# Performance work log

Hardware: AMD Instinct MI355X
Metric: run time of the kernel (lower is better)

## Reference

```python
import jax, jax.numpy as jnp
import numpy as np
import math

B, S, DIM = 2, 2048, 2048
H, KV, HD = 16, 1, 128  # query heads, kv heads, head dim


def setup_inputs() -> dict:
    key = jax.random.key(0)
    ks = jax.random.split(key, 6)
    std = 0.02
    return {
        "hidden_states": jax.random.normal(ks[0], (B, S, DIM), jnp.float32),
        "attention_mask": jnp.zeros((B, 1, S, S), jnp.float32),
        "wq": jax.random.normal(ks[1], (DIM, H * HD), jnp.float32) * std,
        "bq": jnp.zeros((H * HD,), jnp.float32),
        "wk": jax.random.normal(ks[2], (DIM, KV * HD), jnp.float32) * std,
        "bk": jnp.zeros((KV * HD,), jnp.float32),
        "wv": jax.random.normal(ks[3], (DIM, KV * HD), jnp.float32) * std,
        "bv": jnp.zeros((KV * HD,), jnp.float32),
        "wo": jax.random.normal(ks[4], (H * HD, DIM), jnp.float32) * std,
        "bo": jnp.zeros((DIM,), jnp.float32),
    }


def reference(hidden_states, attention_mask, wq, bq, wk, bk, wv, bv, wo, bo):
    b, s, _ = hidden_states.shape
    q = (hidden_states @ wq + bq).reshape(b, s, H, HD)
    k = (hidden_states @ wk + bk).reshape(b, s, KV, HD)
    v = (hidden_states @ wv + bv).reshape(b, s, KV, HD)
    # [b, h, s, d]
    q = jnp.transpose(q, (0, 2, 1, 3))
    k = jnp.transpose(k, (0, 2, 1, 3))
    v = jnp.transpose(v, (0, 2, 1, 3))
    # broadcast shared KV heads to all query heads (num_kv_heads < num_query_heads)
    repeats = H // KV
    k = jnp.repeat(k, repeats, axis=1)
    v = jnp.repeat(v, repeats, axis=1)
    scores = jnp.einsum('bhqd,bhkd->bhqk', q, k) / math.sqrt(HD)
    scores = scores + attention_mask
    weights = jax.nn.softmax(scores, axis=-1)
    attn = jnp.einsum('bhqk,bhkd->bhqd', weights, v)
    attn = jnp.transpose(attn, (0, 2, 1, 3)).reshape(b, s, H * HD)
    return attn @ wo + bo
```

## Files before the change

kernel.cpp:

```cpp
#include <hip/hip_runtime.h>
#include <hip/hip_bf16.h>
#include <stdint.h>

#define S_LEN 2048
#define DIMSZ 2048
#define NH    16
#define HD    128
#define NQK   2176
#define NQKV  2304
#define NT2   (S_LEN / 128)

typedef short  bf16x8  __attribute__((ext_vector_type(8)));
typedef float  floatx4 __attribute__((ext_vector_type(4)));
typedef float  floatx16 __attribute__((ext_vector_type(16)));
typedef int    intx4   __attribute__((ext_vector_type(4)));
typedef unsigned short u16;

#define mfma32 __builtin_amdgcn_mfma_f32_32x32x16_bf16
#define LOG2E 1.4426950408889634f

__device__ __forceinline__ u16 f2bf(float x) {
  unsigned int u = __builtin_bit_cast(unsigned int, x);
  u = (u + 0x7FFFu + ((u >> 16) & 1u)) >> 16;
  return (u16)u;
}

__device__ __forceinline__ int cvtpk(float lo, float hi) {
  int r;
  asm("v_cvt_pk_bf16_f32 %0, %1, %2" : "=v"(r) : "v"(lo), "v"(hi));
  return r;
}

#if __has_builtin(__builtin_amdgcn_exp2f)
__device__ __forceinline__ float fexp2(float x) { return __builtin_amdgcn_exp2f(x); }
#else
__device__ __forceinline__ float fexp2(float x) { return exp2f(x); }
#endif

#if __has_builtin(__builtin_amdgcn_permlane32_swap)
__device__ __forceinline__ void half_swap(int& a, int& b) {
  auto r = __builtin_amdgcn_permlane32_swap(a, b, false, false);
  a = (int)r[0]; b = (int)r[1];
}
__device__ __forceinline__ float red_max32(float x) {
  int xi = __builtin_bit_cast(int, x);
  auto r = __builtin_amdgcn_permlane32_swap(xi, xi, false, false);
  return fmaxf(__builtin_bit_cast(float, (int)r[0]), __builtin_bit_cast(float, (int)r[1]));
}
__device__ __forceinline__ float red_add32(float x) {
  int xi = __builtin_bit_cast(int, x);
  auto r = __builtin_amdgcn_permlane32_swap(xi, xi, false, false);
  return __builtin_bit_cast(float, (int)r[0]) + __builtin_bit_cast(float, (int)r[1]);
}
#else
__device__ __forceinline__ void half_swap(int& a, int& b) {
  int as = __shfl_xor(a, 32);
  int bs = __shfl_xor(b, 32);
  int lane = threadIdx.x & 63;
  int na = (lane < 32) ? a : bs;
  int nb = (lane < 32) ? as : b;
  a = na; b = nb;
}
__device__ __forceinline__ float red_max32(float x) { return fmaxf(x, __shfl_xor(x, 32)); }
__device__ __forceinline__ float red_add32(float x) { return x + __shfl_xor(x, 32); }
#endif

__device__ __forceinline__ void gload16(const void* g, void* l) {
  __builtin_amdgcn_global_load_lds(
      reinterpret_cast<const __attribute__((address_space(1))) void*>(reinterpret_cast<uintptr_t>(g)),
      reinterpret_cast<__attribute__((address_space(3))) void*>(reinterpret_cast<uintptr_t>(l)),
      16, 0, 0);
}

__global__ void k_cvt_bf16(const float* __restrict__ in, u16* __restrict__ out, int n4) {
  int i = blockIdx.x * blockDim.x + threadIdx.x;
  if (i < n4) {
    float4 v = ((const float4*)in)[i];
    ushort4 o;
    o.x = f2bf(v.x); o.y = f2bf(v.y); o.z = f2bf(v.z); o.w = f2bf(v.w);
    ((ushort4*)out)[i] = o;
  }
}

__global__ void k_transpose_bf16(const float* __restrict__ in, u16* __restrict__ out,
                                 int K, int N, int rowOff) {
  __shared__ float t[64][65];
  int c0 = blockIdx.x * 64;
  int r0 = blockIdx.y * 64;
  int tid = threadIdx.x;
  int lr = tid >> 6;
  int lc = tid & 63;
#pragma unroll
  for (int i = 0; i < 16; ++i) {
    int r = lr + i * 4;
    t[r][lc] = in[(size_t)(r0 + r) * N + c0 + lc];
  }
  __syncthreads();
#pragma unroll
  for (int i = 0; i < 16; ++i) {
    int r = lr + i * 4;
    out[(size_t)(rowOff + c0 + r) * K + r0 + lc] = f2bf(t[lc][r]);
  }
}

__global__ void k_bias_concat(const float* __restrict__ bq, const float* __restrict__ bk,
                              const float* __restrict__ bv, float* __restrict__ out) {
  int i = blockIdx.x * 256 + threadIdx.x;
  if (i < NQKV) out[i] = (i < 2048) ? bq[i] : (i < NQK ? bk[i - 2048] : bv[i - NQK]);
}

__device__ __forceinline__ void stage_tile(const u16* __restrict__ G, int ldg, int row0, int kt,
                                           u16* lbase, int wid, int lane) {
#pragma unroll
  for (int i = 0; i < 4; ++i) {
    int c   = (wid * 4 + i) * 64 + lane;
    int row = c >> 3, cin = c & 7;
    int cs  = cin ^ (row & 7);
    const u16* g = G + (size_t)(row0 + row) * ldg + kt * 64 + cs * 8;
    gload16(g, (char*)lbase + (wid * 4 + i) * 1024);
  }
}

template <int OMODE>
__global__ __launch_bounds__(256)
void k_gemm(const u16* __restrict__ A, const u16* __restrict__ Bt,
            const float* __restrict__ bias, void* __restrict__ Cout,
            u16* __restrict__ vt, int M, int N, int K) {
  __shared__ u16 lA[2][128 * 64];
  __shared__ u16 lB[2][128 * 64];
  const int tid = threadIdx.x, lane = tid & 63, wid = tid >> 6;
  const int wm = wid >> 1, wn = wid & 1;
  const int tm = blockIdx.x, tn = blockIdx.y;
  const int nk = K >> 6;

  stage_tile(A, K, tm * 128, 0, lA[0], wid, lane);
  stage_tile(Bt, K, tn * 128, 0, lB[0], wid, lane);
  __syncthreads();

  floatx4 acc[4][4] = {};
  int buf = 0;
  for (int kt = 0; kt < nk; ++kt) {
    if (kt + 1 < nk) {
      stage_tile(A, K, tm * 128, kt + 1, lA[buf ^ 1], wid, lane);
      stage_tile(Bt, K, tn * 128, kt + 1, lB[buf ^ 1], wid, lane);
    }
    const char* pa = (const char*)&lA[buf][0];
    const char* pb = (const char*)&lB[buf][0];
#pragma unroll
    for (int kk = 0; kk < 2; ++kk) {
      bf16x8 af[4], bfr[4];
      int gch = kk * 4 + (lane >> 4);
#pragma unroll
      for (int f = 0; f < 4; ++f) {
        int ra = wm * 64 + f * 16 + (lane & 15);
        af[f]  = *(const bf16x8*)(pa + ra * 128 + ((gch ^ (ra & 7)) << 4));
        int rb = wn * 64 + f * 16 + (lane & 15);
        bfr[f] = *(const bf16x8*)(pb + rb * 128 + ((gch ^ (rb & 7)) << 4));
      }
      __builtin_amdgcn_s_setprio(1);
#pragma unroll
      for (int fm = 0; fm < 4; ++fm)
#pragma unroll
        for (int fn = 0; fn < 4; ++fn)
          acc[fm][fn] = __builtin_amdgcn_mfma_f32_16x16x32_bf16(af[fm], bfr[fn], acc[fm][fn], 0, 0, 0);
      __builtin_amdgcn_s_setprio(0);
    }
    __syncthreads();
    buf ^= 1;
  }

#pragma unroll
  for (int fm = 0; fm < 4; ++fm)
#pragma unroll
    for (int fn = 0; fn < 4; ++fn)
#pragma unroll
      for (int r = 0; r < 4; ++r) {
        int rowg = tm * 128 + wm * 64 + fm * 16 + (lane >> 4) * 4 + r;
        int colg = tn * 128 + wn * 64 + fn * 16 + (lane & 15);
        float v = acc[fm][fn][r] + bias[colg];
        if constexpr (OMODE == 1) {
          ((float*)Cout)[(size_t)rowg * N + colg] = v;
        } else {
          if (colg < NQK) {
            ((u16*)Cout)[(size_t)rowg * N + colg] = f2bf(v);
          } else {
            int d = colg - NQK;
            int bg = rowg >> 11, s = rowg & 2047;
            vt[((size_t)bg * HD + d) * S_LEN + s] = f2bf(v);
          }
        }
      }
}

__device__ __forceinline__ void stage_k128(const u16* __restrict__ qkv, int b, int kt,
                                           u16* lK, int wid, int lane) {
#pragma unroll
  for (int i = 0; i < 4; ++i) {
    int seg = wid * 4 + i;
    int r = seg * 4 + (lane >> 4);
    int cin = lane & 15;
    int cs = cin ^ (r & 15);
    const u16* g = qkv + (size_t)(b * S_LEN + kt * 128 + r) * NQKV + 2048 + cs * 8;
    gload16(g, (char*)lK + seg * 1024);
  }
}
__device__ __forceinline__ void stage_v128(const u16* __restrict__ vt, int b, int kt,
                                           u16* lV, int wid, int lane) {
#pragma unroll
  for (int i = 0; i < 4; ++i) {
    int seg = wid * 4 + i;
    int r = seg * 4 + (lane >> 4);
    int cin = lane & 15;
    int cs = cin ^ (r & 15);
    const u16* g = vt + ((size_t)b * HD + r) * S_LEN + kt * 128 + cs * 8;
    gload16(g, (char*)lV + seg * 1024);
  }
}

__global__ __launch_bounds__(512, 2)
void k_attn(const u16* __restrict__ qkv, const u16* __restrict__ vt,
            const float* __restrict__ mask, u16* __restrict__ attn) {
  __shared__ __align__(16) u16 lK[2][128 * 128];
  __shared__ __align__(16) u16 lV[2][128 * 128];
  const int tid = threadIdx.x, lane = tid & 63, wid = tid >> 6;
  const int qt = blockIdx.x, hg = blockIdx.y, b = blockIdx.z;
  const int h = hg * 8 + wid;
  const int q = lane & 31, h5 = lane >> 5;
  const float scale = 0.08838834764831845f;

  bf16x8 qf[8];
  const size_t qrow = (size_t)(b * S_LEN + qt * 32 + q);
#pragma unroll
  for (int cs = 0; cs < 8; ++cs)
    qf[cs] = *(const bf16x8*)(qkv + qrow * NQKV + h * HD + cs * 16 + h5 * 8);

  int offK[8], offV[8];
#pragma unroll
  for (int cs = 0; cs < 8; ++cs)
    offK[cs] = q * 256 + (((cs * 2 + h5) ^ (q & 15)) << 4);
#pragma unroll
  for (int hf = 0; hf < 2; ++hf)
#pragma unroll
    for (int ks = 0; ks < 4; ++ks)
      offV[hf * 4 + ks] = q * 256 + (((hf * 8 + ks * 2 + h5) ^ (q & 15)) << 4);

  const float* mptr = mask + ((size_t)b * S_LEN + qt * 32 + q) * S_LEN + h5 * 4;

  float m_ = -1e30f, l_ = 0.f;
  floatx16 acco[4] = {};

  stage_k128(qkv, b, 0, lK[0], wid, lane);
  stage_v128(vt, b, 0, lV[0], wid, lane);
  __syncthreads();

  int buf = 0;
  for (int kt = 0; kt < NT2; ++kt) {
    if (kt + 1 < NT2) {
      stage_k128(qkv, b, kt + 1, lK[buf ^ 1], wid, lane);
      stage_v128(vt, b, kt + 1, lV[buf ^ 1], wid, lane);
    }
    const char* pKb = (const char*)&lK[buf][0];
    const char* pVb = (const char*)&lV[buf][0];

#pragma unroll
    for (int half = 0; half < 2; ++half) {
      const float* mh = mptr + kt * 128 + half * 64;
      floatx4 mk[8];
#pragma unroll
      for (int kb = 0; kb < 2; ++kb)
#pragma unroll
        for (int rg = 0; rg < 4; ++rg)
          mk[kb * 4 + rg] = *(const floatx4*)(mh + kb * 32 + rg * 8);

      floatx16 accs0 = {}, accs1 = {};
      const char* pK = pKb + half * 16384;
      __builtin_amdgcn_s_setprio(1);
#pragma unroll
      for (int cs = 0; cs < 8; ++cs) {
        bf16x8 kf0 = *(const bf16x8*)(pK + offK[cs]);
        bf16x8 kf1 = *(const bf16x8*)(pK + 8192 + offK[cs]);
        accs0 = mfma32(kf0, qf[cs], accs0, 0, 0, 0);
        accs1 = mfma32(kf1, qf[cs], accs1, 0, 0, 0);
      }
      __builtin_amdgcn_s_setprio(0);

      float pr[32];
      float pm0 = -1e30f, pm1 = -1e30f, pm2 = -1e30f, pm3 = -1e30f;
#pragma unroll
      for (int kb = 0; kb < 2; ++kb)
#pragma unroll
        for (int rg = 0; rg < 4; ++rg) {
          floatx4 m4 = mk[kb * 4 + rg];
          float s0 = (kb ? accs1[rg * 4 + 0] : accs0[rg * 4 + 0]) * scale + m4[0];
          float s1 = (kb ? accs1[rg * 4 + 1] : accs0[rg * 4 + 1]) * scale + m4[1];
          float s2 = (kb ? accs1[rg * 4 + 2] : accs0[rg * 4 + 2]) * scale + m4[2];
          float s3 = (kb ? accs1[rg * 4 + 3] : accs0[rg * 4 + 3]) * scale + m4[3];
          pr[kb * 16 + rg * 4 + 0] = s0; pm0 = fmaxf(pm0, s0);
          pr[kb * 16 + rg * 4 + 1] = s1; pm1 = fmaxf(pm1, s1);
          pr[kb * 16 + rg * 4 + 2] = s2; pm2 = fmaxf(pm2, s2);
          pr[kb * 16 + rg * 4 + 3] = s3; pm3 = fmaxf(pm3, s3);
        }
      float rowm = red_max32(fmaxf(fmaxf(pm0, pm1), fmaxf(pm2, pm3)));

      if (__any(rowm > m_ + 8.0f)) {
        float mn = fmaxf(m_, rowm);
        float al = fexp2((m_ - mn) * LOG2E);
        m_ = mn;
        l_ *= al;
#pragma unroll
        for (int dt = 0; dt < 4; ++dt) acco[dt] *= al;
      }
      float nml2 = -m_ * LOG2E;
      float ps0 = 0.f, ps1 = 0.f, ps2 = 0.f, ps3 = 0.f;
#pragma unroll
      for (int j = 0; j < 32; j += 4) {
        float e0 = fexp2(pr[j + 0] * LOG2E + nml2); pr[j + 0] = e0; ps0 += e0;
        float e1 = fexp2(pr[j + 1] * LOG2E + nml2); pr[j + 1] = e1; ps1 += e1;
        float e2 = fexp2(pr[j + 2] * LOG2E + nml2); pr[j + 2] = e2; ps2 += e2;
        float e3 = fexp2(pr[j + 3] * LOG2E + nml2); pr[j + 3] = e3; ps3 += e3;
      }
      l_ += red_add32((ps0 + ps1) + (ps2 + ps3));

      bf16x8 pf[4];
#pragma unroll
      for (int kb = 0; kb < 2; ++kb)
#pragma unroll
        for (int s = 0; s < 2; ++s) {
          int base = kb * 16 + s * 8;
          int A0 = cvtpk(pr[base + 0], pr[base + 1]);
          int A1 = cvtpk(pr[base + 2], pr[base + 3]);
          int B0 = cvtpk(pr[base + 4], pr[base + 5]);
          int B1 = cvtpk(pr[base + 6], pr[base + 7]);
          half_swap(A0, B0);
          half_swap(A1, B1);
          intx4 w;
          w[0] = A0; w[1] = A1; w[2] = B0; w[3] = B1;
          pf[kb * 2 + s] = __builtin_bit_cast(bf16x8, w);
        }

      __builtin_amdgcn_s_setprio(1);
#pragma unroll
      for (int dt = 0; dt < 4; ++dt)
#pragma unroll
        for (int ks = 0; ks < 4; ++ks) {
          bf16x8 vf = *(const bf16x8*)(pVb + dt * 8192 + offV[half * 4 + ks]);
          acco[dt] = mfma32(vf, pf[ks], acco[dt], 0, 0, 0);
        }
      __builtin_amdgcn_s_setprio(0);
    }

    __syncthreads();
    buf ^= 1;
  }

  float inv = 1.0f / l_;
  u16* obase = attn + qrow * DIMSZ + h * HD;
#pragma unroll
  for (int dt = 0; dt < 4; ++dt)
#pragma unroll
    for (int rg = 0; rg < 4; ++rg) {
      int d0 = dt * 32 + rg * 8 + h5 * 4;
      ushort4 st;
      st.x = f2bf(acco[dt][rg * 4 + 0] * inv);
      st.y = f2bf(acco[dt][rg * 4 + 1] * inv);
      st.z = f2bf(acco[dt][rg * 4 + 2] * inv);
      st.w = f2bf(acco[dt][rg * 4 + 3] * inv);
      *(ushort4*)(obase + d0) = st;
    }
}

extern "C" void kernel_launch(void* const* d_in, const int* in_sizes, int n_in,
                              void* d_out, int out_size, void* d_ws, size_t ws_size,
                              hipStream_t stream) {
  const float* hidden = (const float*)d_in[0];
  const float* mask   = (const float*)d_in[1];
  const float* wq = (const float*)d_in[2];
  const float* bq = (const float*)d_in[3];
  const float* wk = (const float*)d_in[4];
  const float* bk = (const float*)d_in[5];
  const float* wv = (const float*)d_in[6];
  const float* bv = (const float*)d_in[7];
  const float* wo = (const float*)d_in[8];
  const float* bo = (const float*)d_in[9];
  float* out = (float*)d_out;

  char* ws = (char*)d_ws;
  u16*   hb    = (u16*)(ws);
  u16*   wqkvT = (u16*)(ws + 16777216);
  u16*   woT   = (u16*)(ws + 26214400);
  float* bqkv  = (float*)(ws + 34603008);
  u16*   qkv   = (u16*)(ws + 34612224);
  u16*   vt    = (u16*)(ws + 53486592);
  u16*   attn  = (u16*)(ws + 54535168);

  k_cvt_bf16<<<dim3(8192), dim3(256), 0, stream>>>(hidden, hb, 4096 * 2048 / 4);
  k_transpose_bf16<<<dim3(32, 32), dim3(256), 0, stream>>>(wq, wqkvT, 2048, 2048, 0);
  k_transpose_bf16<<<dim3(2, 32),  dim3(256), 0, stream>>>(wk, wqkvT, 2048, 128, 2048);
  k_transpose_bf16<<<dim3(2, 32),  dim3(256), 0, stream>>>(wv, wqkvT, 2048, 128, NQK);
  k_transpose_bf16<<<dim3(32, 32), dim3(256), 0, stream>>>(wo, woT, 2048, 2048, 0);
  k_bias_concat<<<dim3(9), dim3(256), 0, stream>>>(bq, bk, bv, bqkv);

  k_gemm<0><<<dim3(32, 18), dim3(256), 0, stream>>>(hb, wqkvT, bqkv, (void*)qkv, vt, 4096, NQKV, 2048);
  k_attn<<<dim3(64, 2, 2), dim3(512), 0, stream>>>(qkv, vt, mask, attn);
  k_gemm<1><<<dim3(32, 16), dim3(256), 0, stream>>>(attn, woT, bo, (void*)out, (u16*)nullptr, 4096, 2048, 2048);
}
```

Baseline: 216.3 us.

## Stage mask through LDS as bf16, fold log2e scaling, swizzle GEMM grid

The attention kernel now loads the additive mask cooperatively once per block, pre-scaled by log2e and packed to bf16 in a double-buffered LDS tile. Previously each wave read the fp32 mask from global memory separately, so the same rows were fetched by all eight head waves. Scale and log2e are folded into one multiply, which removes per-element multiplies in the exp path. K and V staging are merged into one helper with a narrower XOR swizzle, and the launch-bounds occupancy hint is dropped. The GEMMs switch to a 1D grid whose block index is remapped across eight groups, which changes which tiles run concurrently and may affect cache behaviour across XCDs. The bf16 mask loses precision, which matters only for non-trivial masks.

```diff
diff --git a/kernel.cpp b/kernel.cpp
--- a/kernel.cpp
+++ b/kernel.cpp
@@ -23,6 +23,9 @@
   unsigned int u = __builtin_bit_cast(unsigned int, x);
   u = (u + 0x7FFFu + ((u >> 16) & 1u)) >> 16;
   return (u16)u;
+}
+__device__ __forceinline__ float bf2f(unsigned int bits) {
+  return __builtin_bit_cast(float, bits << 16);
 }
 
 __device__ __forceinline__ int cvtpk(float lo, float hi) {
@@ -130,7 +133,11 @@
   __shared__ u16 lB[2][128 * 64];
   const int tid = threadIdx.x, lane = tid & 63, wid = tid >> 6;
   const int wm = wid >> 1, wn = wid & 1;
-  const int tm = blockIdx.x, tn = blockIdx.y;
+  const int tmN = M >> 7;
+  const int nwg = tmN * (N >> 7);
+  const int qx = nwg >> 3;
+  const int swz = (blockIdx.x & 7) * qx + (blockIdx.x >> 3);
+  const int tm = swz % tmN, tn = swz / tmN;
   const int nk = K >> 6;
 
   stage_tile(A, K, tm * 128, 0, lA[0], wid, lane);
@@ -192,41 +199,41 @@
       }
 }
 
-__device__ __forceinline__ void stage_k128(const u16* __restrict__ qkv, int b, int kt,
-                                           u16* lK, int wid, int lane) {
+__device__ __forceinline__ void stage_kv128(const u16* __restrict__ qkv, const u16* __restrict__ vt,
+                                            int b, int kt, u16* lK, u16* lV, int wid, int lane) {
 #pragma unroll
   for (int i = 0; i < 4; ++i) {
     int seg = wid * 4 + i;
     int r = seg * 4 + (lane >> 4);
     int cin = lane & 15;
-    int cs = cin ^ (r & 15);
-    const u16* g = qkv + (size_t)(b * S_LEN + kt * 128 + r) * NQKV + 2048 + cs * 8;
-    gload16(g, (char*)lK + seg * 1024);
-  }
-}
-__device__ __forceinline__ void stage_v128(const u16* __restrict__ vt, int b, int kt,
-                                           u16* lV, int wid, int lane) {
-#pragma unroll
-  for (int i = 0; i < 4; ++i) {
-    int seg = wid * 4 + i;
-    int r = seg * 4 + (lane >> 4);
-    int cin = lane & 15;
-    int cs = cin ^ (r & 15);
-    const u16* g = vt + ((size_t)b * HD + r) * S_LEN + kt * 128 + cs * 8;
-    gload16(g, (char*)lV + seg * 1024);
-  }
-}
-
-__global__ __launch_bounds__(512, 2)
+    int cs = cin ^ (r & 7);
+    const u16* gk = qkv + (size_t)(b * S_LEN + kt * 128 + r) * NQKV + 2048 + cs * 8;
+    gload16(gk, (char*)lK + seg * 1024);
+    const u16* gv = vt + ((size_t)b * HD + r) * S_LEN + kt * 128 + cs * 8;
+    gload16(gv, (char*)lV + seg * 1024);
+  }
+}
+
+__device__ __forceinline__ void mask_write128(u16* lMb, int mq, int mc, floatx4 m0, floatx4 m1) {
+  intx4 w;
+  w[0] = cvtpk(m0[0] * LOG2E, m0[1] * LOG2E);
+  w[1] = cvtpk(m0[2] * LOG2E, m0[3] * LOG2E);
+  w[2] = cvtpk(m1[0] * LOG2E, m1[1] * LOG2E);
+  w[3] = cvtpk(m1[2] * LOG2E, m1[3] * LOG2E);
+  *(intx4*)((char*)lMb + mq * 256 + ((mc ^ (mq & 7)) << 4)) = w;
+}
+
+__global__ __launch_bounds__(512)
 void k_attn(const u16* __restrict__ qkv, const u16* __restrict__ vt,
             const float* __restrict__ mask, u16* __restrict__ attn) {
   __shared__ __align__(16) u16 lK[2][128 * 128];
   __shared__ __align__(16) u16 lV[2][128 * 128];
+  __shared__ __align__(16) u16 lMb[2][32 * 128];
   const int tid = threadIdx.x, lane = tid & 63, wid = tid >> 6;
   const int qt = blockIdx.x, hg = blockIdx.y, b = blockIdx.z;
   const int h = hg * 8 + wid;
   const int q = lane & 31, h5 = lane >> 5;
-  const float scale = 0.08838834764831845f;
+  const float c_sl2 = 0.08838834764831845f * LOG2E;
 
   bf16x8 qf[8];
   const size_t qrow = (size_t)(b * S_LEN + qt * 32 + q);
@@ -234,46 +241,47 @@
   for (int cs = 0; cs < 8; ++cs)
     qf[cs] = *(const bf16x8*)(qkv + qrow * NQKV + h * HD + cs * 16 + h5 * 8);
 
-  int offK[8], offV[8];
+  const int qb = q * 256;
+  int offK[8], offVc[8];
 #pragma unroll
   for (int cs = 0; cs < 8; ++cs)
-    offK[cs] = q * 256 + (((cs * 2 + h5) ^ (q & 15)) << 4);
+    offK[cs] = qb + (((cs * 2 + h5) ^ (q & 7)) << 4);
 #pragma unroll
   for (int hf = 0; hf < 2; ++hf)
 #pragma unroll
     for (int ks = 0; ks < 4; ++ks)
-      offV[hf * 4 + ks] = q * 256 + (((hf * 8 + ks * 2 + h5) ^ (q & 15)) << 4);
-
-  const float* mptr = mask + ((size_t)b * S_LEN + qt * 32 + q) * S_LEN + h5 * 4;
+      offVc[hf * 4 + ks] = (((hf * 8 + ks * 2 + h5) ^ (q & 7)) << 4);
 
   float m_ = -1e30f, l_ = 0.f;
   floatx16 acco[4] = {};
 
-  stage_k128(qkv, b, 0, lK[0], wid, lane);
-  stage_v128(vt, b, 0, lV[0], wid, lane);
+  const int mq = tid >> 4, mc = tid & 15;
+  const float* mrow = mask + (size_t)b * S_LEN * S_LEN + (size_t)(qt * 32 + mq) * S_LEN + mc * 8;
+
+  stage_kv128(qkv, vt, b, 0, lK[0], lV[0], wid, lane);
+  {
+    floatx4 m0 = *(const floatx4*)(mrow);
+    floatx4 m1 = *(const floatx4*)(mrow + 4);
+    mask_write128(&lMb[0][0], mq, mc, m0, m1);
+  }
   __syncthreads();
 
   int buf = 0;
   for (int kt = 0; kt < NT2; ++kt) {
+    floatx4 mr0, mr1;
     if (kt + 1 < NT2) {
-      stage_k128(qkv, b, kt + 1, lK[buf ^ 1], wid, lane);
-      stage_v128(vt, b, kt + 1, lV[buf ^ 1], wid, lane);
+      stage_kv128(qkv, vt, b, kt + 1, lK[buf ^ 1], lV[buf ^ 1], wid, lane);
+      mr0 = *(const floatx4*)(mrow + (size_t)(kt + 1) * 128);
+      mr1 = *(const floatx4*)(mrow + (size_t)(kt + 1) * 128 + 4);
     }
     const char* pKb = (const char*)&lK[buf][0];
     const char* pVb = (const char*)&lV[buf][0];
-
-#pragma unroll
-    for (int half = 0; half < 2; ++half) {
-      const float* mh = mptr + kt * 128 + half * 64;
-      floatx4 mk[8];
-#pragma unroll
-      for (int kb = 0; kb < 2; ++kb)
-#pragma unroll
-        for (int rg = 0; rg < 4; ++rg)
-          mk[kb * 4 + rg] = *(const floatx4*)(mh + kb * 32 + rg * 8);
-
+    const char* pMb = (const char*)&lMb[buf][0];
+
+#pragma unroll
+    for (int hf = 0; hf < 2; ++hf) {
       floatx16 accs0 = {}, accs1 = {};
-      const char* pK = pKb + half * 16384;
+      const char* pK = pKb + hf * 16384;
       __builtin_amdgcn_s_setprio(1);
 #pragma unroll
       for (int cs = 0; cs < 8; ++cs) {
@@ -290,11 +298,12 @@
       for (int kb = 0; kb < 2; ++kb)
 #pragma unroll
         for (int rg = 0; rg < 4; ++rg) {
-          floatx4 m4 = mk[kb * 4 + rg];
-          float s0 = (kb ? accs1[rg * 4 + 0] : accs0[rg * 4 + 0]) * scale + m4[0];
-          float s1 = (kb ? accs1[rg * 4 + 1] : accs0[rg * 4 + 1]) * scale + m4[1];
-          float s2 = (kb ? accs1[rg * 4 + 2] : accs0[rg * 4 + 2]) * scale + m4[2];
-          float s3 = (kb ? accs1[rg * 4 + 3] : accs0[rg * 4 + 3]) * scale + m4[3];
+          ushort4 mu = *(const ushort4*)(pMb + qb +
+                         (((hf * 8 + kb * 4 + rg) ^ (q & 7)) << 4) + h5 * 8);
+          float s0 = (kb ? accs1[rg * 4 + 0] : accs0[rg * 4 + 0]) * c_sl2 + bf2f(mu.x);
+          float s1 = (kb ? accs1[rg * 4 + 1] : accs0[rg * 4 + 1]) * c_sl2 + bf2f(mu.y);
+          float s2 = (kb ? accs1[rg * 4 + 2] : accs0[rg * 4 + 2]) * c_sl2 + bf2f(mu.z);
+          float s3 = (kb ? accs1[rg * 4 + 3] : accs0[rg * 4 + 3]) * c_sl2 + bf2f(mu.w);
           pr[kb * 16 + rg * 4 + 0] = s0; pm0 = fmaxf(pm0, s0);
           pr[kb * 16 + rg * 4 + 1] = s1; pm1 = fmaxf(pm1, s1);
           pr[kb * 16 + rg * 4 + 2] = s2; pm2 = fmaxf(pm2, s2);
@@ -302,22 +311,21 @@
         }
       float rowm = red_max32(fmaxf(fmaxf(pm0, pm1), fmaxf(pm2, pm3)));
 
-      if (__any(rowm > m_ + 8.0f)) {
+      if (__any(rowm > m_ + 11.5415603f)) {
         float mn = fmaxf(m_, rowm);
-        float al = fexp2((m_ - mn) * LOG2E);
+        float al = fexp2(m_ - mn);
         m_ = mn;
         l_ *= al;
 #pragma unroll
         for (int dt = 0; dt < 4; ++dt) acco[dt] *= al;
       }
-      float nml2 = -m_ * LOG2E;
       float ps0 = 0.f, ps1 = 0.f, ps2 = 0.f, ps3 = 0.f;
 #pragma unroll
       for (int j = 0; j < 32; j += 4) {
-        float e0 = fexp2(pr[j + 0] * LOG2E + nml2); pr[j + 0] = e0; ps0 += e0;
-        float e1 = fexp2(pr[j + 1] * LOG2E + nml2); pr[j + 1] = e1; ps1 += e1;
-        float e2 = fexp2(pr[j + 2] * LOG2E + nml2); pr[j + 2] = e2; ps2 += e2;
-        float e3 = fexp2(pr[j + 3] * LOG2E + nml2); pr[j + 3] = e3; ps3 += e3;
+        float e0 = fexp2(pr[j + 0] - m_); pr[j + 0] = e0; ps0 += e0;
+        float e1 = fexp2(pr[j + 1] - m_); pr[j + 1] = e1; ps1 += e1;
+        float e2 = fexp2(pr[j + 2] - m_); pr[j + 2] = e2; ps2 += e2;
+        float e3 = fexp2(pr[j + 3] - m_); pr[j + 3] = e3; ps3 += e3;
       }
       l_ += red_add32((ps0 + ps1) + (ps2 + ps3));
 
@@ -343,12 +351,14 @@
       for (int dt = 0; dt < 4; ++dt)
 #pragma unroll
         for (int ks = 0; ks < 4; ++ks) {
-          bf16x8 vf = *(const bf16x8*)(pVb + dt * 8192 + offV[half * 4 + ks]);
+          bf16x8 vf = *(const bf16x8*)(pVb + dt * 8192 + qb + offVc[hf * 4 + ks]);
           acco[dt] = mfma32(vf, pf[ks], acco[dt], 0, 0, 0);
         }
       __builtin_amdgcn_s_setprio(0);
     }
 
+    if (kt + 1 < NT2)
+      mask_write128(&lMb[buf ^ 1][0], mq, mc, mr0, mr1);
     __syncthreads();
     buf ^= 1;
   }
@@ -400,7 +410,7 @@
   k_transpose_bf16<<<dim3(32, 32), dim3(256), 0, stream>>>(wo, woT, 2048, 2048, 0);
   k_bias_concat<<<dim3(9), dim3(256), 0, stream>>>(bq, bk, bv, bqkv);
 
-  k_gemm<0><<<dim3(32, 18), dim3(256), 0, stream>>>(hb, wqkvT, bqkv, (void*)qkv, vt, 4096, NQKV, 2048);
+  k_gemm<0><<<dim3(576), dim3(256), 0, stream>>>(hb, wqkvT, bqkv, (void*)qkv, vt, 4096, NQKV, 2048);
   k_attn<<<dim3(64, 2, 2), dim3(512), 0, stream>>>(qkv, vt, mask, attn);
-  k_gemm<1><<<dim3(32, 16), dim3(256), 0, stream>>>(attn, woT, bo, (void*)out, (u16*)nullptr, 4096, 2048, 2048);
-}
+  k_gemm<1><<<dim3(512), dim3(256), 0, stream>>>(attn, woT, bo, (void*)out, (u16*)nullptr, 4096, 2048, 2048);
+}
```

After: 213.7 us. Within noise of the previous version (-1.2%).
